# Kernel tuning notes

Hardware: AMD Instinct MI355X
Metric: run time of the kernel (lower is better)

Reference implementation:

```python
import jax, jax.numpy as jnp
import numpy as np
from jax import lax

B, C, H, W = 64, 3, 224, 224
P, NP, D, HEADS, DEPTH = 16, 196, 384, 6, 6
DD, DHEADS, DDEPTH = 256, 8, 4
NVIS = 49


def setup_inputs():
    key = jax.random.key(0)
    ks = iter(jax.random.split(key, 64))
    def rn(shape, s=0.02):
        return jax.random.normal(next(ks), shape, jnp.float32) * s
    perms = jax.vmap(lambda k: jax.random.permutation(k, NP))(jax.random.split(next(ks), B))
    inp = {
        'x': jax.random.normal(next(ks), (B, C, H, W), jnp.float32),
        'unmasked_idx': perms[:, :NVIS].astype(jnp.int32),
        'masked_idx': perms[:, NVIS:].astype(jnp.int32),
        'conv_w': rn((D, C, P, P)), 'conv_b': jnp.zeros((D,), jnp.float32),
        'cls_token': rn((D,)), 'pos_embed': rn((NP + 1, D)),
        'enc_ln1_w': jnp.ones((DEPTH, D), jnp.float32), 'enc_ln1_b': jnp.zeros((DEPTH, D), jnp.float32),
        'enc_qkv_w': rn((DEPTH, 3 * D, D)), 'enc_qkv_b': jnp.zeros((DEPTH, 3 * D), jnp.float32),
        'enc_out_w': rn((DEPTH, D, D)), 'enc_out_b': jnp.zeros((DEPTH, D), jnp.float32),
        'enc_ln2_w': jnp.ones((DEPTH, D), jnp.float32), 'enc_ln2_b': jnp.zeros((DEPTH, D), jnp.float32),
        'enc_fc1_w': rn((DEPTH, 4 * D, D)), 'enc_fc1_b': jnp.zeros((DEPTH, 4 * D), jnp.float32),
        'enc_fc2_w': rn((DEPTH, D, 4 * D)), 'enc_fc2_b': jnp.zeros((DEPTH, D), jnp.float32),
        'enc_norm_w': jnp.ones((D,), jnp.float32), 'enc_norm_b': jnp.zeros((D,), jnp.float32),
        'dec_embed_w': rn((DD, D)), 'dec_embed_b': jnp.zeros((DD,), jnp.float32),
        'mask_token': rn((DD,)), 'dec_pos_embed': rn((NP + 1, DD)),
        'dec_ln1_w': jnp.ones((DDEPTH, DD), jnp.float32), 'dec_ln1_b': jnp.zeros((DDEPTH, DD), jnp.float32),
        'dec_qkv_w': rn((DDEPTH, 3 * DD, DD)), 'dec_qkv_b': jnp.zeros((DDEPTH, 3 * DD), jnp.float32),
        'dec_out_w': rn((DDEPTH, DD, DD)), 'dec_out_b': jnp.zeros((DDEPTH, DD), jnp.float32),
        'dec_ln2_w': jnp.ones((DDEPTH, DD), jnp.float32), 'dec_ln2_b': jnp.zeros((DDEPTH, DD), jnp.float32),
        'dec_fc1_w': rn((DDEPTH, 4 * DD, DD)), 'dec_fc1_b': jnp.zeros((DDEPTH, 4 * DD), jnp.float32),
        'dec_fc2_w': rn((DDEPTH, DD, 4 * DD)), 'dec_fc2_b': jnp.zeros((DDEPTH, DD), jnp.float32),
        'dec_norm_w': jnp.ones((DD,), jnp.float32), 'dec_norm_b': jnp.zeros((DD,), jnp.float32),
        'pred_w': rn((P * P * 3, DD)), 'pred_b': jnp.zeros((P * P * 3,), jnp.float32),
    }
    return inp


def layer_norm(x, w, b, eps=1e-5):
    m = x.mean(-1, keepdims=True)
    v = ((x - m) ** 2).mean(-1, keepdims=True)
    return (x - m) * lax.rsqrt(v + eps) * w + b


def mha(x, wqkv, bqkv, wo, bo, h):
    b, s, d = x.shape
    dh = d // h
    qkv = x @ wqkv.T + bqkv
    q, k, v = jnp.split(qkv, 3, axis=-1)
    sp = lambda t: t.reshape(b, s, h, dh).transpose(0, 2, 1, 3)  # [b,h,s,dh]
    q, k, v = sp(q), sp(k), sp(v)
    scores = jnp.einsum('bhqd,bhkd->bhqk', q, k) * (1.0 / np.sqrt(dh))
    a = jax.nn.softmax(scores, axis=-1)
    o = jnp.einsum('bhqk,bhkd->bhqd', a, v).transpose(0, 2, 1, 3).reshape(b, s, d)
    return o @ wo.T + bo


def run_blocks(x, depth, heads, ln1_w, ln1_b, qkv_w, qkv_b, out_w, out_b, ln2_w, ln2_b, fc1_w, fc1_b, fc2_w, fc2_b):
    for i in range(depth):
        x = x + mha(layer_norm(x, ln1_w[i], ln1_b[i]), qkv_w[i], qkv_b[i], out_w[i], out_b[i], heads)
        hdn = jax.nn.gelu(layer_norm(x, ln2_w[i], ln2_b[i]) @ fc1_w[i].T + fc1_b[i], approximate=False)
        x = x + hdn @ fc2_w[i].T + fc2_b[i]
    return x


def reference(x, unmasked_idx, masked_idx, conv_w, conv_b, cls_token, pos_embed,
              enc_ln1_w, enc_ln1_b, enc_qkv_w, enc_qkv_b, enc_out_w, enc_out_b,
              enc_ln2_w, enc_ln2_b, enc_fc1_w, enc_fc1_b, enc_fc2_w, enc_fc2_b,
              enc_norm_w, enc_norm_b, dec_embed_w, dec_embed_b, mask_token, dec_pos_embed,
              dec_ln1_w, dec_ln1_b, dec_qkv_w, dec_qkv_b, dec_out_w, dec_out_b,
              dec_ln2_w, dec_ln2_b, dec_fc1_w, dec_fc1_b, dec_fc2_w, dec_fc2_b,
              dec_norm_w, dec_norm_b, pred_w, pred_b):
    b = x.shape[0]
    # patch embed: conv stride=kernel=16 -> [B, D, 14, 14] -> [B, 196, D]
    p = lax.conv_general_dilated(x, conv_w, (P, P), 'VALID',
                                 dimension_numbers=('NCHW', 'OIHW', 'NCHW'))
    p = p.reshape(b, D, NP).transpose(0, 2, 1) + conv_b + pos_embed[1:]
    bi = jnp.arange(b)[:, None]
    vis = p[bi, unmasked_idx]                      # [B, NVIS, D] per-sample gather
    cls = cls_token + pos_embed[0]
    xe = jnp.concatenate([jnp.broadcast_to(cls, (b, 1, D)), vis], axis=1)
    xe = run_blocks(xe, DEPTH, HEADS, enc_ln1_w, enc_ln1_b, enc_qkv_w, enc_qkv_b,
                    enc_out_w, enc_out_b, enc_ln2_w, enc_ln2_b, enc_fc1_w, enc_fc1_b,
                    enc_fc2_w, enc_fc2_b)
    xe = layer_norm(xe, enc_norm_w, enc_norm_b)
    xd = xe @ dec_embed_w.T + dec_embed_b          # [B, 1+NVIS, DD]
    vis_dec = xd[:, 1:, :]                         # drop cls
    full = jnp.zeros((b, NP, DD), xd.dtype)
    full = full.at[bi, unmasked_idx].set(vis_dec)  # scatter visible tokens
    full = full.at[bi, masked_idx].set(mask_token) # scatter mask tokens
    full = full + dec_pos_embed[1:]
    xf = run_blocks(full, DDEPTH, DHEADS, dec_ln1_w, dec_ln1_b, dec_qkv_w, dec_qkv_b,
                    dec_out_w, dec_out_b, dec_ln2_w, dec_ln2_b, dec_fc1_w, dec_fc1_b,
                    dec_fc2_w, dec_fc2_b)
    xf = layer_norm(xf, dec_norm_w, dec_norm_b)
    return xf @ pred_w.T + pred_b                  # [B, NP, P*P*3]
```

## Files before the change

kernel.cpp:

```cpp
#include <hip/hip_runtime.h>
#include <hip/hip_bf16.h>

#define B_    64
#define NP_   196
#define NVIS_ 49
#define D_    384
#define DD_   256
#define SENC_ 50
#define SDEC_ 196

typedef __hip_bfloat16 bf16;
typedef __attribute__((ext_vector_type(8))) short short8;
typedef __attribute__((ext_vector_type(4))) float float4v;

__device__ __forceinline__ float bf2f(bf16 x) { return __bfloat162float(x); }
__device__ __forceinline__ bf16 f2bf(float x) { return __float2bfloat16(x); }
__device__ __forceinline__ float rdin(const void* p, long i, int f) {
  return f ? ((const float*)p)[i] : bf2f(((const bf16*)p)[i]);
}

__global__ void probe_kernel(const void* w, int* flag) {
  int tid = threadIdx.x;
  float mx = 0.f;
  for (int i = tid; i < 512; i += 64)
    mx = fmaxf(mx, fabsf(bf2f(((const bf16*)w)[i])));
#pragma unroll
  for (int off = 32; off; off >>= 1) mx = fmaxf(mx, __shfl_xor(mx, off));
  if (tid == 0) *flag = (mx > 1e3f) ? 1 : 0;
}

__global__ __launch_bounds__(256) void fill_kernel(bf16* out, float v, int n) {
  int idx = blockIdx.x * 256 + threadIdx.x;
  if (idx < n) out[idx] = f2bf(v);
}

__global__ __launch_bounds__(256) void im2col_vis_kernel(
    const void* __restrict__ x, const int* __restrict__ unmasked,
    bf16* __restrict__ out, const int* __restrict__ dflag) {
  int f = *dflag;
  int idx = blockIdx.x * 256 + threadIdx.x;
  const int TOT = B_ * NVIS_ * 768;
  if (idx >= TOT) return;
  int k = idx % 768;
  int row = idx / 768;
  int j = row % NVIS_;
  int b = row / NVIS_;
  int n = unmasked[b * NVIS_ + j];
  int ph = n / 14, pw = n % 14;
  int c  = k >> 8;
  int rr = (k >> 4) & 15;
  int cc = k & 15;
  out[idx] = f2bf(rdin(x, (long)(((b * 3 + c) * 224) + ph * 16 + rr) * 224 + pw * 16 + cc, f));
}

#define LDK2 72
#define UNR _Pragma("unroll")
template <int MODE, int TMW, int TNW>
__global__ __launch_bounds__(256) void gemm_kernel(
    const bf16* __restrict__ A, const void* __restrict__ W, long wOff,
    const void* __restrict__ bias, long bOff,
    void* __restrict__ C, int M, int N, int K, int KS, int out_mode,
    const int* __restrict__ dflag) {
  constexpr int BM = 2 * TMW, BN = 2 * TNW;
  constexpr int AM = TMW / 16, AN = TNW / 16;
  constexpr int AR = BM / 32, BR = BN / 32;
  int f = *dflag;
  __shared__ bf16 Asl[2][BM * LDK2];
  __shared__ bf16 Bsl[2][BN * LDK2];
  int tid = threadIdx.x;

  int gx = gridDim.x;
  int nwg = gx * gridDim.y;
  int orig = blockIdx.y * gx + blockIdx.x;
  int q = nwg >> 3, rr_ = nwg & 7, xcd = orig & 7, off = orig >> 3;
  int wgid = (xcd < rr_ ? xcd * (q + 1) : rr_ * (q + 1) + (xcd - rr_) * q) + off;
  int bx = wgid % gx, by = wgid / gx, bz = blockIdx.z;

  int w = tid >> 6, lane = tid & 63;
  int quad = lane >> 4, l16 = lane & 15;
  int wm = (w & 1) * TMW, wn = (w >> 1) * TNW;
  int rstg = tid >> 3, cstg = (tid & 7) * 8;
  const bf16* Ab = A + (long)by * BM * K + (long)rstg * K + cstg;
  int k0lo = bz * KS;

  float4v acc[AM][AN];
#pragma unroll
  for (int i = 0; i < AM; i++)
#pragma unroll
    for (int j = 0; j < AN; j++) acc[i][j] = (float4v){0.f, 0.f, 0.f, 0.f};

#define LOAD_A(k0) UNR for (int i = 0; i < AR; i++) \
    apre[i] = *(const uint4*)(Ab + (long)i * 32 * K + (k0));
#define STORE_A(buf) UNR for (int i = 0; i < AR; i++) \
    *(uint4*)(&Asl[buf][(rstg + i * 32) * LDK2 + cstg]) = apre[i];
#define LOAD_BF(k0) UNR for (int i = 0; i < BR; i++) { \
    const float* p_ = Wf + (long)i * 32 * K + (k0); \
    blo[i] = *(const uint4*)p_; bhi[i] = *(const uint4*)(p_ + 4); }
#define STORE_BF(buf) UNR for (int i = 0; i < BR; i++) { \
    union { uint4 u; float ff[4]; } lo_, hi_; lo_.u = blo[i]; hi_.u = bhi[i]; \
    union { uint4 u; bf16 hh[8]; } pk_; \
    pk_.hh[0] = f2bf(lo_.ff[0]); pk_.hh[1] = f2bf(lo_.ff[1]); \
    pk_.hh[2] = f2bf(lo_.ff[2]); pk_.hh[3] = f2bf(lo_.ff[3]); \
    pk_.hh[4] = f2bf(hi_.ff[0]); pk_.hh[5] = f2bf(hi_.ff[1]); \
    pk_.hh[6] = f2bf(hi_.ff[2]); pk_.hh[7] = f2bf(hi_.ff[3]); \
    *(uint4*)(&Bsl[buf][(rstg + i * 32) * LDK2 + cstg]) = pk_.u; }
#define LOAD_BH(k0) UNR for (int i = 0; i < BR; i++) \
    blo[i] = *(const uint4*)(Wh + (long)i * 32 * K + (k0));
#define STORE_BH(buf) UNR for (int i = 0; i < BR; i++) \
    *(uint4*)(&Bsl[buf][(rstg + i * 32) * LDK2 + cstg]) = blo[i];
#define COMPUTE(cur) UNR for (int kk = 0; kk < 2; kk++) { \
    short8 af[AM], bfr[AN]; \
    UNR for (int mi = 0; mi < AM; mi++) \
      af[mi] = *(const short8*)&Asl[cur][(wm + mi * 16 + l16) * LDK2 + kk * 32 + quad * 8]; \
    UNR for (int ni = 0; ni < AN; ni++) \
      bfr[ni] = *(const short8*)&Bsl[cur][(wn + ni * 16 + l16) * LDK2 + kk * 32 + quad * 8]; \
    UNR for (int mi = 0; mi < AM; mi++) \
      UNR for (int ni = 0; ni < AN; ni++) \
        acc[mi][ni] = __builtin_amdgcn_mfma_f32_16x16x32_bf16( \
            af[mi], bfr[ni], acc[mi][ni], 0, 0, 0); }

  int nst = KS >> 6;
  if (f) {
    const float* Wf = (const float*)W + wOff + (long)bx * BN * K + (long)rstg * K + cstg;
    uint4 apre[AR], blo[BR], bhi[BR];
    LOAD_A(k0lo); LOAD_BF(k0lo);
    STORE_A(0);   STORE_BF(0);
    __syncthreads();
    for (int s = 0; s < nst - 1; s++) {
      int cur = s & 1;
      int k0 = k0lo + (s + 1) * 64;
      LOAD_A(k0); LOAD_BF(k0);
      COMPUTE(cur);
      STORE_A(cur ^ 1); STORE_BF(cur ^ 1);
      __syncthreads();
    }
    COMPUTE((nst - 1) & 1);
  } else {
    const bf16* Wh = (const bf16*)W + wOff + (long)bx * BN * K + (long)rstg * K + cstg;
    uint4 apre[AR], blo[BR];
    LOAD_A(k0lo); LOAD_BH(k0lo);
    STORE_A(0);   STORE_BH(0);
    __syncthreads();
    for (int s = 0; s < nst - 1; s++) {
      int cur = s & 1;
      int k0 = k0lo + (s + 1) * 64;
      LOAD_A(k0); LOAD_BH(k0);
      COMPUTE(cur);
      STORE_A(cur ^ 1); STORE_BH(cur ^ 1);
      __syncthreads();
    }
    COMPUTE((nst - 1) & 1);
  }
#undef LOAD_A
#undef STORE_A
#undef LOAD_BF
#undef STORE_BF
#undef LOAD_BH
#undef STORE_BH
#undef COMPUTE

  int om = (out_mode == 2) ? (f ? 1 : 0) : out_mode;
  float* Cf = (float*)C + (long)bz * M * N;
  bf16*  Cb = (bf16*)C;
#pragma unroll
  for (int mi = 0; mi < AM; mi++) {
#pragma unroll
    for (int ni = 0; ni < AN; ni++) {
      int cn = bx * BN + wn + ni * 16 + l16;
      float bval = (bz == 0) ? rdin(bias, bOff + cn, f) : 0.f;
#pragma unroll
      for (int r = 0; r < 4; r++) {
        int cm = by * BM + wm + mi * 16 + quad * 4 + r;
        float v = acc[mi][ni][r] + bval;
        if constexpr (MODE == 1) v = 0.5f * v * (1.0f + erff(v * 0.70710678f));
        if (om) Cf[(long)cm * N + cn] = v;
        else    Cb[(long)cm * N + cn] = f2bf(v);
      }
    }
  }
}

template <int N>
__global__ __launch_bounds__(256) void ln_kernel(
    float* __restrict__ X, const float* __restrict__ G0,
    const float* __restrict__ G1, const float* __restrict__ G2,
    const void* __restrict__ w, long wOff, const void* __restrict__ bv,
    long bOff, bf16* __restrict__ Y, int M, const int* __restrict__ dflag) {
  int f = *dflag;
  int row = blockIdx.x * 4 + (threadIdx.x >> 6);
  int lane = threadIdx.x & 63;
  if (row >= M) return;
  float* xr = X + (long)row * N;
  const float* g0 = G0 ? G0 + (long)row * N : nullptr;
  const float* g1 = G1 ? G1 + (long)row * N : nullptr;
  const float* g2 = G2 ? G2 + (long)row * N : nullptr;
  constexpr int CNT = N / 64;
  float v[CNT];
  float sum = 0.f;
#pragma unroll
  for (int i = 0; i < CNT; i++) {
    int c = lane + 64 * i;
    float t = xr[c];
    if (g0) t += g0[c];
    if (g1) t += g1[c];
    if (g2) t += g2[c];
    if (g0) xr[c] = t;
    v[i] = t;
    sum += t;
  }
#pragma unroll
  for (int off = 32; off; off >>= 1) sum += __shfl_xor(sum, off);
  float mean = sum * (1.0f / N);
  float vs = 0.f;
#pragma unroll
  for (int i = 0; i < CNT; i++) { float d = v[i] - mean; vs += d * d; }
#pragma unroll
  for (int off = 32; off; off >>= 1) vs += __shfl_xor(vs, off);
  float rstd = rsqrtf(vs * (1.0f / N) + 1e-5f);
  bf16* yr = Y + (long)row * N;
#pragma unroll
  for (int i = 0; i < CNT; i++) {
    int cidx = lane + 64 * i;
    yr[cidx] = f2bf((v[i] - mean) * rstd * rdin(w, wOff + cidx, f) + rdin(bv, bOff + cidx, f));
  }
}

__global__ __launch_bounds__(256) void attn_dec_kernel(
    const bf16* __restrict__ qkv, bf16* __restrict__ out) {
  const int S = SDEC_, DH = 32, Dm = 256, tri = 768;
  const int KLD = 40, VLD = 232, PLD = 232;
  int b = blockIdx.x >> 3, h = blockIdx.x & 7;
  __shared__ bf16 Ksh[208 * KLD];
  __shared__ bf16 Vt[32 * VLD];
  __shared__ bf16 Psh[4][16 * PLD];
  int tid = threadIdx.x;
  const bf16* base = qkv + (long)b * S * tri;
  for (int idx = tid; idx < S * 4; idx += 256) {
    int s = idx >> 2, part = (idx & 3) * 8;
    uint4 v = *(const uint4*)(base + (long)s * tri + Dm + h * DH + part);
    *(uint4*)(&Ksh[s * KLD + part]) = v;
  }
  if (tid < 12 * 4) {
    int s = 196 + (tid >> 2), part = (tid & 3) * 8;
    uint4 z = {0, 0, 0, 0};
    *(uint4*)(&Ksh[s * KLD + part]) = z;
  }
  for (int idx = tid; idx < S * DH; idx += 256) {
    int s = idx >> 5, d = idx & 31;
    Vt[d * VLD + s] = base[(long)s * tri + 2 * Dm + h * DH + d];
  }
  for (int idx = tid; idx < 32 * 36; idx += 256) {
    int d = idx / 36, c = 196 + idx % 36;
    Vt[d * VLD + c] = f2bf(0.f);
  }
  __syncthreads();
  int w = tid >> 6, lane = tid & 63, l16 = lane & 15, quad = lane >> 4;
  bf16* Pw = &Psh[w][0];
  const float scale = 0.17677669529663687f;
  for (int qt = w; qt < 13; qt += 4) {
    int q0 = qt * 16;
    int qr = min(q0 + l16, S - 1);
    short8 qf = *(const short8*)(base + (long)qr * tri + h * DH + quad * 8);
    float4v sc[13];
#pragma unroll
    for (int t = 0; t < 13; t++) {
      short8 kf = *(const short8*)&Ksh[(t * 16 + l16) * KLD + quad * 8];
      sc[t] = __builtin_amdgcn_mfma_f32_16x16x32_bf16(
          qf, kf, (float4v){0.f, 0.f, 0.f, 0.f}, 0, 0, 0);
    }
    float mx[4] = {-1e30f, -1e30f, -1e30f, -1e30f};
#pragma unroll
    for (int t = 0; t < 13; t++) {
      bool valid = (t * 16 + l16) < S;
#pragma unroll
      for (int r = 0; r < 4; r++) {
        float v = valid ? sc[t][r] * scale : -1e30f;
        sc[t][r] = v;
        mx[r] = fmaxf(mx[r], v);
      }
    }
#pragma unroll
    for (int off = 1; off < 16; off <<= 1)
#pragma unroll
      for (int r = 0; r < 4; r++) mx[r] = fmaxf(mx[r], __shfl_xor(mx[r], off));
    float sm[4] = {0.f, 0.f, 0.f, 0.f};
#pragma unroll
    for (int t = 0; t < 13; t++)
#pragma unroll
      for (int r = 0; r < 4; r++) {
        float p = __expf(sc[t][r] - mx[r]);
        sc[t][r] = p;
        sm[r] += p;
      }
#pragma unroll
    for (int off = 1; off < 16; off <<= 1)
#pragma unroll
      for (int r = 0; r < 4; r++) sm[r] += __shfl_xor(sm[r], off);
#pragma unroll
    for (int t = 0; t < 14; t++) {
      int col = t * 16 + l16;
#pragma unroll
      for (int r = 0; r < 4; r++) {
        float p = (t < 13) ? sc[t][r] : 0.f;
        Pw[(quad * 4 + r) * PLD + col] = f2bf(p);
      }
    }
    __asm__ volatile("s_waitcnt lgkmcnt(0)" ::: "memory");
    float4v o0 = {0.f, 0.f, 0.f, 0.f}, o1 = {0.f, 0.f, 0.f, 0.f};
#pragma unroll
    for (int kc = 0; kc < 7; kc++) {
      short8 pf = *(const short8*)&Pw[l16 * PLD + kc * 32 + quad * 8];
      short8 v0 = *(const short8*)&Vt[l16 * VLD + kc * 32 + quad * 8];
      short8 v1 = *(const short8*)&Vt[(16 + l16) * VLD + kc * 32 + quad * 8];
      o0 = __builtin_amdgcn_mfma_f32_16x16x32_bf16(pf, v0, o0, 0, 0, 0);
      o1 = __builtin_amdgcn_mfma_f32_16x16x32_bf16(pf, v1, o1, 0, 0, 0);
    }
#pragma unroll
    for (int r = 0; r < 4; r++) {
      int row = q0 + quad * 4 + r;
      if (row < S) {
        float inv = 1.f / sm[r];
        bf16* op = out + ((long)(b * S + row)) * Dm + h * DH;
        op[l16]      = f2bf(o0[r] * inv);
        op[16 + l16] = f2bf(o1[r] * inv);
      }
    }
  }
}

__global__ __launch_bounds__(128) void attn_enc_kernel(
    const bf16* __restrict__ qkv, bf16* __restrict__ out) {
  const int S = SENC_, H = 6, DH = 64, Dm = H * DH, tri = 3 * Dm;
  int b = blockIdx.x / H, h = blockIdx.x % H;
  int tid = threadIdx.x;
  __shared__ float Ks[SENC_ * 64];
  __shared__ float Vs[SENC_ * 64];
  __shared__ float P1[SENC_ * 66];
  const bf16* base = qkv + (long)b * S * tri;
  for (int idx = tid; idx < S * 8; idx += 128) {
    int s = idx >> 3, part = (idx & 7) * 8;
    union { uint4 u; bf16 hh[8]; } kk, vv;
    kk.u = *(const uint4*)(base + (long)s * tri + Dm + h * DH + part);
    vv.u = *(const uint4*)(base + (long)s * tri + 2 * Dm + h * DH + part);
#pragma unroll
    for (int j = 0; j < 8; j++) {
      Ks[s * DH + part + j] = bf2f(kk.hh[j]);
      Vs[s * DH + part + j] = bf2f(vv.hh[j]);
    }
  }
  __syncthreads();
  int w = tid >> 6, lane = tid & 63;
  int row = lane;
  float q[DH], o[DH];
  float m = -1e30f, l = 0.f;
  if (lane < S) {
    const float scale = 0.125f;
#pragma unroll
    for (int d = 0; d < DH; d++) {
      q[d] = bf2f(base[(long)row * tri + h * DH + d]) * scale;
      o[d] = 0.f;
    }
    int jlo = w * 25, jhi = jlo + 25;
    for (int j = jlo; j < jhi; j++) {
      float s = 0.f;
#pragma unroll
      for (int d = 0; d < DH; d++) s += q[d] * Ks[j * DH + d];
      float mn = fmaxf(m, s);
      float corr = __expf(m - mn);
      float p = __expf(s - mn);
      l = l * corr + p;
      m = mn;
#pragma unroll
      for (int d = 0; d < DH; d++) o[d] = o[d] * corr + p * Vs[j * DH + d];
    }
    if (w == 1) {
#pragma unroll
      for (int d = 0; d < DH; d++) P1[row * 66 + d] = o[d];
      P1[row * 66 + 64] = m;
      P1[row * 66 + 65] = l;
    }
  }
  __syncthreads();
  if (w == 0 && lane < S) {
    float m1 = P1[row * 66 + 64], l1 = P1[row * 66 + 65];
    float mg = fmaxf(m, m1);
    float e0 = __expf(m - mg), e1 = __expf(m1 - mg);
    float lg = l * e0 + l1 * e1;
    float inv = 1.f / lg;
    bf16* op = out + ((long)(b * S + row) * Dm + h * DH);
#pragma unroll
    for (int d = 0; d < DH; d++)
      op[d] = f2bf((o[d] * e0 + P1[row * 66 + d] * e1) * inv);
  }
}

__global__ __launch_bounds__(256) void build_xe_kernel(
    const float* __restrict__ G0, const float* __restrict__ G1,
    const float* __restrict__ G2, const void* __restrict__ cls,
    const void* __restrict__ pos, const int* __restrict__ unmasked,
    float* __restrict__ xe, const int* __restrict__ dflag) {
  int f = *dflag;
  int idx = blockIdx.x * 256 + threadIdx.x;
  const int TOT = B_ * SENC_ * D_;
  if (idx >= TOT) return;
  int d = idx % D_;
  int s = (idx / D_) % SENC_;
  int b = idx / (D_ * SENC_);
  float v;
  if (s == 0) {
    v = rdin(cls, d, f) + rdin(pos, d, f);
  } else {
    int j = s - 1;
    int n = unmasked[b * NVIS_ + j];
    long r = (long)(b * NVIS_ + j) * D_ + d;
    v = G0[r] + G1[r] + G2[r] + rdin(pos, (long)(1 + n) * D_ + d, f);
  }
  xe[idx] = v;
}

__global__ __launch_bounds__(256) void dec_init_kernel(
    const void* __restrict__ mask_token, const void* __restrict__ dpos,
    float* __restrict__ full, const int* __restrict__ dflag) {
  int f = *dflag;
  int idx = blockIdx.x * 256 + threadIdx.x;
  const int TOT = B_ * NP_ * DD_;
  if (idx >= TOT) return;
  int d = idx % DD_;
  int n = (idx / DD_) % NP_;
  full[idx] = rdin(mask_token, d, f) + rdin(dpos, (long)(1 + n) * DD_ + d, f);
}

__global__ __launch_bounds__(256) void dec_scatter_kernel(
    const float* __restrict__ Gx0, const float* __restrict__ Gx1,
    const int* __restrict__ unmasked, const void* __restrict__ dpos,
    float* __restrict__ full, const int* __restrict__ dflag) {
  int f = *dflag;
  int idx = blockIdx.x * 256 + threadIdx.x;
  const int TOT = B_ * NVIS_ * DD_;
  if (idx >= TOT) return;
  int d = idx % DD_;
  int j = (idx / DD_) % NVIS_;
  int b = idx / (DD_ * NVIS_);
  int n = unmasked[b * NVIS_ + j];
  long r = (long)(b * SENC_ + 1 + j) * DD_ + d;
  full[((long)(b * NP_ + n)) * DD_ + d] =
      Gx0[r] + Gx1[r] + rdin(dpos, (long)(1 + n) * DD_ + d, f);
}

extern "C" void kernel_launch(void* const* d_in, const int* in_sizes, int n_in,
                              void* d_out, int out_size, void* d_ws, size_t ws_size,
                              hipStream_t stream) {
  (void)in_sizes; (void)n_in;
  const int* unmasked = (const int*)d_in[1];
  const int M_ENC = B_ * SENC_;
  const int M_DEC = B_ * NP_;

  const size_t NEEDED = 58884100;
  if (ws_size < NEEDED) {
    fill_kernel<<<(out_size + 255) / 256, 256, 0, stream>>>(
        (bf16*)d_out, (float)(ws_size >> 20), out_size);
    return;
  }
  char* wsb = (char*)d_ws;
  bf16*  big    = (bf16*)wsb;
  float* full   = (float*)(wsb + 25690112);
  bf16*  im2col = (bf16*)(wsb + 25690112);
  bf16*  t0     = (bf16*)(wsb + 38535168);
  float* xe     = (float*)(wsb + 44957696);
  float* Gdec   = (float*)(wsb + 44957696);
  int*   dflag  = (int*)(wsb + 58884096);
  float* Gp0 = (float*)(wsb + 0);
  float* Gp1 = (float*)(wsb + 4915200);
  float* Gp2 = (float*)(wsb + 9830400);
  float* Gf0 = (float*)(wsb + 9830400);
  float* Gf1 = (float*)(wsb + 14745600);
  float* Gf2 = (float*)(wsb + 19660800);
  float* Gx0 = (float*)(wsb + 0);
  float* Gx1 = (float*)(wsb + 3276800);

  probe_kernel<<<1, 64, 0, stream>>>(d_in[3], dflag);

  auto gemm = [&](int mode, int cfg, const bf16* A, const void* W, long wOff,
                  const void* bias, long bOff, void* C,
                  int M, int N, int K, int splits, int out_mode) {
    int BM = (cfg == 2) ? 64 : 128;
    int BN = (cfg == 0) ? 128 : 64;
    dim3 g(N / BN, M / BM, splits);
    int KS = K / splits;
#define GL(MO, TM, TN) gemm_kernel<MO, TM, TN><<<g, 256, 0, stream>>>( \
        A, W, wOff, bias, bOff, C, M, N, K, KS, out_mode, dflag)
    if (mode == 0) {
      if (cfg == 0) GL(0, 64, 64); else if (cfg == 1) GL(0, 64, 32); else GL(0, 32, 32);
    } else {
      if (cfg == 0) GL(1, 64, 64); else if (cfg == 1) GL(1, 64, 32); else GL(1, 32, 32);
    }
#undef GL
  };

  {
    int tot = B_ * NVIS_ * 768;
    im2col_vis_kernel<<<(tot + 255) / 256, 256, 0, stream>>>(d_in[0], unmasked, im2col, dflag);
    gemm(0, 2, im2col, d_in[3], 0, d_in[4], 0, Gp0, 3200, D_, 768, 3, 1);
    int tot2 = B_ * SENC_ * D_;
    build_xe_kernel<<<(tot2 + 255) / 256, 256, 0, stream>>>(
        Gp0, Gp1, Gp2, d_in[5], d_in[6], unmasked, xe, dflag);
  }

  const float *eg0 = nullptr, *eg1 = nullptr, *eg2 = nullptr;
  for (int i = 0; i < 6; i++) {
    ln_kernel<D_><<<M_ENC / 4, 256, 0, stream>>>(
        xe, eg0, eg1, eg2, d_in[7], (long)i * D_, d_in[8], (long)i * D_, t0, M_ENC, dflag);
    gemm(0, 2, t0, d_in[9], (long)i * 3 * D_ * D_, d_in[10], (long)i * 3 * D_, big, M_ENC, 3 * D_, D_, 1, 0);
    attn_enc_kernel<<<B_ * 6, 128, 0, stream>>>(big, t0);
    gemm(0, 2, t0, d_in[11], (long)i * D_ * D_, d_in[12], (long)i * D_, Gp0, M_ENC, D_, D_, 2, 1);
    ln_kernel<D_><<<M_ENC / 4, 256, 0, stream>>>(
        xe, Gp0, Gp1, nullptr, d_in[13], (long)i * D_, d_in[14], (long)i * D_, t0, M_ENC, dflag);
    gemm(1, 2, t0, d_in[15], (long)i * 4 * D_ * D_, d_in[16], (long)i * 4 * D_, big, M_ENC, 4 * D_, D_, 1, 0);
    gemm(0, 2, big, d_in[17], (long)i * D_ * 4 * D_, d_in[18], (long)i * D_, Gf0, M_ENC, D_, 4 * D_, 3, 1);
    eg0 = Gf0; eg1 = Gf1; eg2 = Gf2;
  }
  ln_kernel<D_><<<M_ENC / 4, 256, 0, stream>>>(
      xe, Gf0, Gf1, Gf2, d_in[19], 0, d_in[20], 0, t0, M_ENC, dflag);
  gemm(0, 2, t0, d_in[21], 0, d_in[22], 0, Gx0, M_ENC, DD_, D_, 2, 1);

  {
    int tot = B_ * NP_ * DD_;
    dec_init_kernel<<<(tot + 255) / 256, 256, 0, stream>>>(d_in[23], d_in[24], full, dflag);
    int tot2 = B_ * NVIS_ * DD_;
    dec_scatter_kernel<<<(tot2 + 255) / 256, 256, 0, stream>>>(
        Gx0, Gx1, unmasked, d_in[24], full, dflag);
  }

  const float* dg = nullptr;
  for (int i = 0; i < 4; i++) {
    ln_kernel<DD_><<<M_DEC / 4, 256, 0, stream>>>(
        full, dg, nullptr, nullptr, d_in[25], (long)i * DD_, d_in[26], (long)i * DD_, t0, M_DEC, dflag);
    gemm(0, 1, t0, d_in[27], (long)i * 3 * DD_ * DD_, d_in[28], (long)i * 3 * DD_, big, M_DEC, 3 * DD_, DD_, 1, 0);
    attn_dec_kernel<<<B_ * 8, 256, 0, stream>>>(big, t0);
    gemm(0, 2, t0, d_in[29], (long)i * DD_ * DD_, d_in[30], (long)i * DD_, Gdec, M_DEC, DD_, DD_, 1, 1);
    ln_kernel<DD_><<<M_DEC / 4, 256, 0, stream>>>(
        full, Gdec, nullptr, nullptr, d_in[31], (long)i * DD_, d_in[32], (long)i * DD_, t0, M_DEC, dflag);
    gemm(1, 0, t0, d_in[33], (long)i * 4 * DD_ * DD_, d_in[34], (long)i * DD_ * 4, big, M_DEC, 4 * DD_, DD_, 1, 0);
    gemm(0, 2, big, d_in[35], (long)i * DD_ * 4 * DD_, d_in[36], (long)i * DD_, Gdec, M_DEC, DD_, 4 * DD_, 1, 1);
    dg = Gdec;
  }
  ln_kernel<DD_><<<M_DEC / 4, 256, 0, stream>>>(
      full, Gdec, nullptr, nullptr, d_in[37], 0, d_in[38], 0, t0, M_DEC, dflag);

  gemm(0, 1, t0, d_in[39], 0, d_in[40], 0, d_out, M_DEC, 768, DD_, 1, 2);
}
```

Baseline: 1.369 ms.

## Pre-convert weights to bf16 and stage GEMM tiles via direct global-to-LDS loads

Adds a one-shot kernel that converts all weight tensors into a bf16 workspace copy at the start of each call, so the GEMM no longer carries an fp32 conversion path. The GEMM now stages A and W tiles with global_load_lds 16-byte transfers into unpadded 64-wide LDS rows, using an XOR swizzle in place of padding to avoid bank conflicts, and the loop now issues the next tile load before computing. The decoder FC1 drops the 128x128 tile config for 128x64. This adds a full weight conversion pass per call and a larger workspace.

```diff
diff --git a/kernel.cpp b/kernel.cpp
--- a/kernel.cpp
+++ b/kernel.cpp
@@ -18,6 +18,11 @@
 __device__ __forceinline__ float rdin(const void* p, long i, int f) {
   return f ? ((const float*)p)[i] : bf2f(((const bf16*)p)[i]);
 }
+__device__ __forceinline__ void gll16(const bf16* g, bf16* l) {
+  __builtin_amdgcn_global_load_lds(
+      (const __attribute__((address_space(1))) unsigned int*)g,
+      (__attribute__((address_space(3))) unsigned int*)l, 16, 0, 0);
+}
 
 __global__ void probe_kernel(const void* w, int* flag) {
   int tid = threadIdx.x;
@@ -32,6 +37,27 @@
 __global__ __launch_bounds__(256) void fill_kernel(bf16* out, float v, int n) {
   int idx = blockIdx.x * 256 + threadIdx.x;
   if (idx < n) out[idx] = f2bf(v);
+}
+
+struct WLs { const void* s[11]; long d[11]; int n[11]; };
+__global__ __launch_bounds__(256) void wconv_kernel(WLs L, bf16* Wb,
+                                                    const int* dflag) {
+  int f = *dflag;
+  int seg = blockIdx.y;
+  long n8 = (long)(L.n[seg] >> 3);
+  long i = (long)blockIdx.x * 256 + threadIdx.x;
+  if (i >= n8) return;
+  bf16* d = Wb + L.d[seg] + i * 8;
+  if (f) {
+    const float4* s = (const float4*)L.s[seg] + i * 2;
+    float4 a = s[0], b = s[1];
+    union { uint4 u; bf16 h[8]; } pk;
+    pk.h[0] = f2bf(a.x); pk.h[1] = f2bf(a.y); pk.h[2] = f2bf(a.z); pk.h[3] = f2bf(a.w);
+    pk.h[4] = f2bf(b.x); pk.h[5] = f2bf(b.y); pk.h[6] = f2bf(b.z); pk.h[7] = f2bf(b.w);
+    *(uint4*)d = pk.u;
+  } else {
+    *(uint4*)d = ((const uint4*)L.s[seg])[i];
+  }
 }
 
 __global__ __launch_bounds__(256) void im2col_vis_kernel(
@@ -53,20 +79,19 @@
   out[idx] = f2bf(rdin(x, (long)(((b * 3 + c) * 224) + ph * 16 + rr) * 224 + pw * 16 + cc, f));
 }
 
-#define LDK2 72
 #define UNR _Pragma("unroll")
 template <int MODE, int TMW, int TNW>
 __global__ __launch_bounds__(256) void gemm_kernel(
-    const bf16* __restrict__ A, const void* __restrict__ W, long wOff,
+    const bf16* __restrict__ A, const bf16* __restrict__ W,
     const void* __restrict__ bias, long bOff,
     void* __restrict__ C, int M, int N, int K, int KS, int out_mode,
     const int* __restrict__ dflag) {
   constexpr int BM = 2 * TMW, BN = 2 * TNW;
   constexpr int AM = TMW / 16, AN = TNW / 16;
-  constexpr int AR = BM / 32, BR = BN / 32;
-  int f = *dflag;
-  __shared__ bf16 Asl[2][BM * LDK2];
-  __shared__ bf16 Bsl[2][BN * LDK2];
+  constexpr int ACH = BM / 32, BCH = BN / 32;
+  int f = *dflag;
+  __shared__ bf16 Asl[2][BM * 64];
+  __shared__ bf16 Bsl[2][BN * 64];
   int tid = threadIdx.x;
 
   int gx = gridDim.x;
@@ -78,9 +103,13 @@
 
   int w = tid >> 6, lane = tid & 63;
   int quad = lane >> 4, l16 = lane & 15;
+  int rb = l16 & 7;
   int wm = (w & 1) * TMW, wn = (w >> 1) * TNW;
-  int rstg = tid >> 3, cstg = (tid & 7) * 8;
-  const bf16* Ab = A + (long)by * BM * K + (long)rstg * K + cstg;
+  int srow = tid >> 3;
+  int dcol = (tid & 7) * 8;
+  int scol = (((tid & 7) ^ (srow & 7))) * 8;
+  const bf16* Ab = A + (long)by * BM * K;
+  const bf16* Wp = W + (long)bx * BN * K;
   int k0lo = bz * KS;
 
   float4v acc[AM][AN];
@@ -89,74 +118,35 @@
 #pragma unroll
     for (int j = 0; j < AN; j++) acc[i][j] = (float4v){0.f, 0.f, 0.f, 0.f};
 
-#define LOAD_A(k0) UNR for (int i = 0; i < AR; i++) \
-    apre[i] = *(const uint4*)(Ab + (long)i * 32 * K + (k0));
-#define STORE_A(buf) UNR for (int i = 0; i < AR; i++) \
-    *(uint4*)(&Asl[buf][(rstg + i * 32) * LDK2 + cstg]) = apre[i];
-#define LOAD_BF(k0) UNR for (int i = 0; i < BR; i++) { \
-    const float* p_ = Wf + (long)i * 32 * K + (k0); \
-    blo[i] = *(const uint4*)p_; bhi[i] = *(const uint4*)(p_ + 4); }
-#define STORE_BF(buf) UNR for (int i = 0; i < BR; i++) { \
-    union { uint4 u; float ff[4]; } lo_, hi_; lo_.u = blo[i]; hi_.u = bhi[i]; \
-    union { uint4 u; bf16 hh[8]; } pk_; \
-    pk_.hh[0] = f2bf(lo_.ff[0]); pk_.hh[1] = f2bf(lo_.ff[1]); \
-    pk_.hh[2] = f2bf(lo_.ff[2]); pk_.hh[3] = f2bf(lo_.ff[3]); \
-    pk_.hh[4] = f2bf(hi_.ff[0]); pk_.hh[5] = f2bf(hi_.ff[1]); \
-    pk_.hh[6] = f2bf(hi_.ff[2]); pk_.hh[7] = f2bf(hi_.ff[3]); \
-    *(uint4*)(&Bsl[buf][(rstg + i * 32) * LDK2 + cstg]) = pk_.u; }
-#define LOAD_BH(k0) UNR for (int i = 0; i < BR; i++) \
-    blo[i] = *(const uint4*)(Wh + (long)i * 32 * K + (k0));
-#define STORE_BH(buf) UNR for (int i = 0; i < BR; i++) \
-    *(uint4*)(&Bsl[buf][(rstg + i * 32) * LDK2 + cstg]) = blo[i];
+#define STAGE(buf, k0) \
+  UNR for (int i_ = 0; i_ < ACH; i_++) { \
+    int r_ = i_ * 32 + srow; \
+    gll16(Ab + (long)r_ * K + (k0) + scol, &Asl[buf][r_ * 64 + dcol]); } \
+  UNR for (int i_ = 0; i_ < BCH; i_++) { \
+    int r_ = i_ * 32 + srow; \
+    gll16(Wp + (long)r_ * K + (k0) + scol, &Bsl[buf][r_ * 64 + dcol]); }
+
 #define COMPUTE(cur) UNR for (int kk = 0; kk < 2; kk++) { \
     short8 af[AM], bfr[AN]; \
     UNR for (int mi = 0; mi < AM; mi++) \
-      af[mi] = *(const short8*)&Asl[cur][(wm + mi * 16 + l16) * LDK2 + kk * 32 + quad * 8]; \
+      af[mi] = *(const short8*)&Asl[cur][(wm + mi * 16 + l16) * 64 + ((kk * 4 + quad) ^ rb) * 8]; \
     UNR for (int ni = 0; ni < AN; ni++) \
-      bfr[ni] = *(const short8*)&Bsl[cur][(wn + ni * 16 + l16) * LDK2 + kk * 32 + quad * 8]; \
+      bfr[ni] = *(const short8*)&Bsl[cur][(wn + ni * 16 + l16) * 64 + ((kk * 4 + quad) ^ rb) * 8]; \
     UNR for (int mi = 0; mi < AM; mi++) \
       UNR for (int ni = 0; ni < AN; ni++) \
         acc[mi][ni] = __builtin_amdgcn_mfma_f32_16x16x32_bf16( \
             af[mi], bfr[ni], acc[mi][ni], 0, 0, 0); }
 
+  STAGE(0, k0lo);
+  __syncthreads();
   int nst = KS >> 6;
-  if (f) {
-    const float* Wf = (const float*)W + wOff + (long)bx * BN * K + (long)rstg * K + cstg;
-    uint4 apre[AR], blo[BR], bhi[BR];
-    LOAD_A(k0lo); LOAD_BF(k0lo);
-    STORE_A(0);   STORE_BF(0);
+  for (int s = 0; s < nst; s++) {
+    int cur = s & 1;
+    if (s + 1 < nst) STAGE(cur ^ 1, k0lo + (s + 1) * 64);
+    COMPUTE(cur);
     __syncthreads();
-    for (int s = 0; s < nst - 1; s++) {
-      int cur = s & 1;
-      int k0 = k0lo + (s + 1) * 64;
-      LOAD_A(k0); LOAD_BF(k0);
-      COMPUTE(cur);
-      STORE_A(cur ^ 1); STORE_BF(cur ^ 1);
-      __syncthreads();
-    }
-    COMPUTE((nst - 1) & 1);
-  } else {
-    const bf16* Wh = (const bf16*)W + wOff + (long)bx * BN * K + (long)rstg * K + cstg;
-    uint4 apre[AR], blo[BR];
-    LOAD_A(k0lo); LOAD_BH(k0lo);
-    STORE_A(0);   STORE_BH(0);
-    __syncthreads();
-    for (int s = 0; s < nst - 1; s++) {
-      int cur = s & 1;
-      int k0 = k0lo + (s + 1) * 64;
-      LOAD_A(k0); LOAD_BH(k0);
-      COMPUTE(cur);
-      STORE_A(cur ^ 1); STORE_BH(cur ^ 1);
-      __syncthreads();
-    }
-    COMPUTE((nst - 1) & 1);
-  }
-#undef LOAD_A
-#undef STORE_A
-#undef LOAD_BF
-#undef STORE_BF
-#undef LOAD_BH
-#undef STORE_BH
+  }
+#undef STAGE
 #undef COMPUTE
 
   int om = (out_mode == 2) ? (f ? 1 : 0) : out_mode;
@@ -455,7 +445,7 @@
   const int M_ENC = B_ * SENC_;
   const int M_DEC = B_ * NP_;
 
-  const size_t NEEDED = 58884100;
+  const size_t NEEDED = 87588880;
   if (ws_size < NEEDED) {
     fill_kernel<<<(out_size + 255) / 256, 256, 0, stream>>>(
         (bf16*)d_out, (float)(ws_size >> 20), out_size);
@@ -469,6 +459,7 @@
   float* xe     = (float*)(wsb + 44957696);
   float* Gdec   = (float*)(wsb + 44957696);
   int*   dflag  = (int*)(wsb + 58884096);
+  bf16*  Wb     = (bf16*)(wsb + 58884112);
   float* Gp0 = (float*)(wsb + 0);
   float* Gp1 = (float*)(wsb + 4915200);
   float* Gp2 = (float*)(wsb + 9830400);
@@ -478,29 +469,48 @@
   float* Gx0 = (float*)(wsb + 0);
   float* Gx1 = (float*)(wsb + 3276800);
 
+  const long o_conv = 0,        o_eqkv = 294912,  o_eout = 2949120;
+  const long o_efc1 = 3833856,  o_efc2 = 7372800, o_demb = 10911744;
+  const long o_dqkv = 11010048, o_dout = 11796480, o_dfc1 = 12058624;
+  const long o_dfc2 = 13107200, o_pred = 14155776;
+
   probe_kernel<<<1, 64, 0, stream>>>(d_in[3], dflag);
-
-  auto gemm = [&](int mode, int cfg, const bf16* A, const void* W, long wOff,
+  {
+    WLs L;
+    L.s[0] = d_in[3];  L.d[0] = o_conv; L.n[0] = 294912;
+    L.s[1] = d_in[9];  L.d[1] = o_eqkv; L.n[1] = 2654208;
+    L.s[2] = d_in[11]; L.d[2] = o_eout; L.n[2] = 884736;
+    L.s[3] = d_in[15]; L.d[3] = o_efc1; L.n[3] = 3538944;
+    L.s[4] = d_in[17]; L.d[4] = o_efc2; L.n[4] = 3538944;
+    L.s[5] = d_in[21]; L.d[5] = o_demb; L.n[5] = 98304;
+    L.s[6] = d_in[27]; L.d[6] = o_dqkv; L.n[6] = 786432;
+    L.s[7] = d_in[29]; L.d[7] = o_dout; L.n[7] = 262144;
+    L.s[8] = d_in[33]; L.d[8] = o_dfc1; L.n[8] = 1048576;
+    L.s[9] = d_in[35]; L.d[9] = o_dfc2; L.n[9] = 1048576;
+    L.s[10] = d_in[39]; L.d[10] = o_pred; L.n[10] = 196608;
+    dim3 g((3538944 / 8 + 255) / 256, 11);
+    wconv_kernel<<<g, 256, 0, stream>>>(L, Wb, dflag);
+  }
+
+  auto gemm = [&](int mode, int cfg, const bf16* A, const bf16* Wp,
                   const void* bias, long bOff, void* C,
                   int M, int N, int K, int splits, int out_mode) {
     int BM = (cfg == 2) ? 64 : 128;
-    int BN = (cfg == 0) ? 128 : 64;
-    dim3 g(N / BN, M / BM, splits);
+    dim3 g(N / 64, M / BM, splits);
     int KS = K / splits;
-#define GL(MO, TM, TN) gemm_kernel<MO, TM, TN><<<g, 256, 0, stream>>>( \
-        A, W, wOff, bias, bOff, C, M, N, K, KS, out_mode, dflag)
     if (mode == 0) {
-      if (cfg == 0) GL(0, 64, 64); else if (cfg == 1) GL(0, 64, 32); else GL(0, 32, 32);
+      if (cfg == 1) gemm_kernel<0, 64, 32><<<g, 256, 0, stream>>>(A, Wp, bias, bOff, C, M, N, K, KS, out_mode, dflag);
+      else          gemm_kernel<0, 32, 32><<<g, 256, 0, stream>>>(A, Wp, bias, bOff, C, M, N, K, KS, out_mode, dflag);
     } else {
-      if (cfg == 0) GL(1, 64, 64); else if (cfg == 1) GL(1, 64, 32); else GL(1, 32, 32);
-    }
-#undef GL
+      if (cfg == 1) gemm_kernel<1, 64, 32><<<g, 256, 0, stream>>>(A, Wp, bias, bOff, C, M, N, K, KS, out_mode, dflag);
+      else          gemm_kernel<1, 32, 32><<<g, 256, 0, stream>>>(A, Wp, bias, bOff, C, M, N, K, KS, out_mode, dflag);
+    }
   };
 
   {
     int tot = B_ * NVIS_ * 768;
     im2col_vis_kernel<<<(tot + 255) / 256, 256, 0, stream>>>(d_in[0], unmasked, im2col, dflag);
-    gemm(0, 2, im2col, d_in[3], 0, d_in[4], 0, Gp0, 3200, D_, 768, 3, 1);
+    gemm(0, 2, im2col, Wb + o_conv, d_in[4], 0, Gp0, 3200, D_, 768, 3, 1);
     int tot2 = B_ * SENC_ * D_;
     build_xe_kernel<<<(tot2 + 255) / 256, 256, 0, stream>>>(
         Gp0, Gp1, Gp2, d_in[5], d_in[6], unmasked, xe, dflag);
@@ -510,18 +520,18 @@
   for (int i = 0; i < 6; i++) {
     ln_kernel<D_><<<M_ENC / 4, 256, 0, stream>>>(
         xe, eg0, eg1, eg2, d_in[7], (long)i * D_, d_in[8], (long)i * D_, t0, M_ENC, dflag);
-    gemm(0, 2, t0, d_in[9], (long)i * 3 * D_ * D_, d_in[10], (long)i * 3 * D_, big, M_ENC, 3 * D_, D_, 1, 0);
+    gemm(0, 2, t0, Wb + o_eqkv + (long)i * 3 * D_ * D_, d_in[10], (long)i * 3 * D_, big, M_ENC, 3 * D_, D_, 1, 0);
     attn_enc_kernel<<<B_ * 6, 128, 0, stream>>>(big, t0);
-    gemm(0, 2, t0, d_in[11], (long)i * D_ * D_, d_in[12], (long)i * D_, Gp0, M_ENC, D_, D_, 2, 1);
+    gemm(0, 2, t0, Wb + o_eout + (long)i * D_ * D_, d_in[12], (long)i * D_, Gp0, M_ENC, D_, D_, 2, 1);
     ln_kernel<D_><<<M_ENC / 4, 256, 0, stream>>>(
         xe, Gp0, Gp1, nullptr, d_in[13], (long)i * D_, d_in[14], (long)i * D_, t0, M_ENC, dflag);
-    gemm(1, 2, t0, d_in[15], (long)i * 4 * D_ * D_, d_in[16], (long)i * 4 * D_, big, M_ENC, 4 * D_, D_, 1, 0);
-    gemm(0, 2, big, d_in[17], (long)i * D_ * 4 * D_, d_in[18], (long)i * D_, Gf0, M_ENC, D_, 4 * D_, 3, 1);
+    gemm(1, 2, t0, Wb + o_efc1 + (long)i * 4 * D_ * D_, d_in[16], (long)i * 4 * D_, big, M_ENC, 4 * D_, D_, 1, 0);
+    gemm(0, 2, big, Wb + o_efc2 + (long)i * D_ * 4 * D_, d_in[18], (long)i * D_, Gf0, M_ENC, D_, 4 * D_, 3, 1);
     eg0 = Gf0; eg1 = Gf1; eg2 = Gf2;
   }
   ln_kernel<D_><<<M_ENC / 4, 256, 0, stream>>>(
       xe, Gf0, Gf1, Gf2, d_in[19], 0, d_in[20], 0, t0, M_ENC, dflag);
-  gemm(0, 2, t0, d_in[21], 0, d_in[22], 0, Gx0, M_ENC, DD_, D_, 2, 1);
+  gemm(0, 2, t0, Wb + o_demb, d_in[22], 0, Gx0, M_ENC, DD_, D_, 2, 1);
 
   {
     int tot = B_ * NP_ * DD_;
@@ -535,17 +545,17 @@
   for (int i = 0; i < 4; i++) {
     ln_kernel<DD_><<<M_DEC / 4, 256, 0, stream>>>(
         full, dg, nullptr, nullptr, d_in[25], (long)i * DD_, d_in[26], (long)i * DD_, t0, M_DEC, dflag);
-    gemm(0, 1, t0, d_in[27], (long)i * 3 * DD_ * DD_, d_in[28], (long)i * 3 * DD_, big, M_DEC, 3 * DD_, DD_, 1, 0);
+    gemm(0, 1, t0, Wb + o_dqkv + (long)i * 3 * DD_ * DD_, d_in[28], (long)i * 3 * DD_, big, M_DEC, 3 * DD_, DD_, 1, 0);
     attn_dec_kernel<<<B_ * 8, 256, 0, stream>>>(big, t0);
-    gemm(0, 2, t0, d_in[29], (long)i * DD_ * DD_, d_in[30], (long)i * DD_, Gdec, M_DEC, DD_, DD_, 1, 1);
+    gemm(0, 2, t0, Wb + o_dout + (long)i * DD_ * DD_, d_in[30], (long)i * DD_, Gdec, M_DEC, DD_, DD_, 1, 1);
     ln_kernel<DD_><<<M_DEC / 4, 256, 0, stream>>>(
         full, Gdec, nullptr, nullptr, d_in[31], (long)i * DD_, d_in[32], (long)i * DD_, t0, M_DEC, dflag);
-    gemm(1, 0, t0, d_in[33], (long)i * 4 * DD_ * DD_, d_in[34], (long)i * DD_ * 4, big, M_DEC, 4 * DD_, DD_, 1, 0);
-    gemm(0, 2, big, d_in[35], (long)i * DD_ * 4 * DD_, d_in[36], (long)i * DD_, Gdec, M_DEC, DD_, 4 * DD_, 1, 1);
+    gemm(1, 1, t0, Wb + o_dfc1 + (long)i * 4 * DD_ * DD_, d_in[34], (long)i * 4 * DD_, big, M_DEC, 4 * DD_, DD_, 1, 0);
+    gemm(0, 2, big, Wb + o_dfc2 + (long)i * DD_ * 4 * DD_, d_in[36], (long)i * DD_, Gdec, M_DEC, DD_, 4 * DD_, 1, 1);
     dg = Gdec;
   }
   ln_kernel<DD_><<<M_DEC / 4, 256, 0, stream>>>(
       full, Gdec, nullptr, nullptr, d_in[37], 0, d_in[38], 0, t0, M_DEC, dflag);
 
-  gemm(0, 1, t0, d_in[39], 0, d_in[40], 0, d_out, M_DEC, 768, DD_, 1, 2);
-}
+  gemm(0, 1, t0, Wb + o_pred, d_in[40], 0, d_out, M_DEC, 768, DD_, 1, 2);
+}
```

Measured after the change: 1.261 ms. -7.9%, faster.
